# Kernel optimization log

Measured on AMD Instinct MI355X. Metric: run time of the kernel, lower is better.

The kernel has to match this reference:

```python
import jax, jax.numpy as jnp
import numpy as np

T, B, D, H = 512, 64, 1024, 1024  # seq_len, batch, input_dim, hidden (out_dim, bi_dir=False)


def setup_inputs() -> dict:
    key = jax.random.key(0)
    k = jax.random.split(key, 5)
    s = 1.0 / np.sqrt(H)  # PyTorch LSTMCell init scale
    x = jax.random.normal(k[0], (T, B, D), dtype=jnp.float32)
    W_ih = jax.random.uniform(k[1], (4 * H, D), minval=-s, maxval=s, dtype=jnp.float32)
    W_hh = jax.random.uniform(k[2], (4 * H, H), minval=-s, maxval=s, dtype=jnp.float32)
    b_ih = jax.random.uniform(k[3], (4 * H,), minval=-s, maxval=s, dtype=jnp.float32)
    b_hh = jax.random.uniform(k[4], (4 * H,), minval=-s, maxval=s, dtype=jnp.float32)
    return {"x": x, "W_ih": W_ih, "W_hh": W_hh, "b_ih": b_ih, "b_hh": b_hh}


def reference(x, W_ih, W_hh, b_ih, b_hh):
    # Unidirectional LSTM over [T, B, D] -> [T, B, H], PyTorch LSTMCell gate order i,f,g,o.
    # Precompute input contribution for all timesteps in one big GEMM.
    xg = jnp.einsum('tbd,gd->tbg', x, W_ih) + b_ih + b_hh  # [T, B, 4H]

    def step(carry, xg_t):
        h, c = carry
        gates = xg_t + h @ W_hh.T  # [B, 4H]
        i, f, g, o = jnp.split(gates, 4, axis=-1)
        c = jax.nn.sigmoid(f) * c + jax.nn.sigmoid(i) * jnp.tanh(g)
        h = jax.nn.sigmoid(o) * jnp.tanh(c)
        return (h, c), h

    h0 = jnp.zeros((B, H), dtype=x.dtype)
    c0 = jnp.zeros((B, H), dtype=x.dtype)
    _, hs = jax.lax.scan(step, (h0, c0), xg)  # hs: [T, B, H]
    return hs
```

## Files before the change

kernel.cpp:

```cpp
#include <hip/hip_runtime.h>
#include <hip/hip_bf16.h>
#include <stdint.h>

#define T_STEPS 512
#define BATCH   64
#define DIM     1024
#define HID     1024
#define NG      4096
#define MROWS   (T_STEPS * BATCH)

typedef __bf16 bf16;
typedef __bf16 bf16x4 __attribute__((ext_vector_type(4)));
typedef __bf16 bf16x8 __attribute__((ext_vector_type(8)));
typedef float  f32x4  __attribute__((ext_vector_type(4)));
typedef unsigned int u32;
typedef u32 u32x2 __attribute__((ext_vector_type(2)));
typedef u32 u32x4 __attribute__((ext_vector_type(4)));

__device__ __forceinline__ void g2lds16(const void* g, void* l) {
    __builtin_amdgcn_global_load_lds(
        (const __attribute__((address_space(1))) void*)g,
        (__attribute__((address_space(3))) void*)l, 16, 0, 0);
}

__device__ __forceinline__ float fsigmoid(float x) {
    return 1.0f / (1.0f + __expf(-x));
}
__device__ __forceinline__ float ftanh_(float x) {
    return 1.0f - 2.0f / (__expf(2.0f * x) + 1.0f);
}

__device__ __forceinline__ u32x4 load16_cc(const void* p) {
    u32x4 r;
    asm volatile("global_load_dwordx4 %0, %1, off sc0 sc1" : "=v"(r) : "v"(p) : "memory");
    return r;
}
__device__ __forceinline__ void store2_cc(void* p, u32 v) {
    asm volatile("global_store_short %0, %1, off sc0 sc1" :: "v"(p), "v"(v) : "memory");
}
__device__ __forceinline__ u32x2 load8_cached(const void* p) {
    u32x2 r;
    asm volatile("global_load_dwordx2 %0, %1, off" : "=v"(r) : "v"(p) : "memory");
    return r;
}
__device__ __forceinline__ void store4_f32(float* p, float v) {
    asm volatile("global_store_dword %0, %1, off" :: "v"(p), "v"(v) : "memory");
}
#define WAITVM(n) asm volatile("s_waitcnt vmcnt(" #n ")" ::: "memory")

__global__ __launch_bounds__(256) void prep_kernel(
    const float* __restrict__ x,   const float* __restrict__ wih,
    const float* __restrict__ whh, const float* __restrict__ bih,
    const float* __restrict__ bhh,
    bf16* __restrict__ xb, bf16* __restrict__ wihp, bf16* __restrict__ wfrag,
    float* __restrict__ bsump, bf16* __restrict__ hbuf, u32* __restrict__ flags)
{
    const int nt  = gridDim.x * blockDim.x;
    const int gid = blockIdx.x * blockDim.x + threadIdx.x;

    for (int i = gid; i < MROWS * DIM / 4; i += nt) {
        f32x4 v = *(const f32x4*)(x + (size_t)i * 4);
        bf16x4 o = {(bf16)v[0], (bf16)v[1], (bf16)v[2], (bf16)v[3]};
        *(bf16x4*)(xb + (size_t)i * 4) = o;
    }
    for (int i = gid; i < NG * (DIM / 4); i += nt) {
        const int n = i >> 8, c4 = (i & 255) * 4;
        f32x4 v = *(const f32x4*)(wih + (size_t)n * DIM + c4);
        bf16x4 o = {(bf16)v[0], (bf16)v[1], (bf16)v[2], (bf16)v[3]};
        const int np = ((n & 1023) << 2) | (n >> 10);
        *(bf16x4*)(wihp + (size_t)np * DIM + c4) = o;
    }
    for (int i = gid; i < NG * HID / 8; i += nt) {
        const int lane = i & 63;
        const int f    = (i >> 6) & 63;
        const int wv   = (i >> 12) & 3;
        const int hg   = i >> 14;
        const int n = f & 7, kk = f >> 3;
        const int grow = (lane & 3) * 1024 + hg * 32 + n * 4 + ((lane & 15) >> 2);
        const int k0   = wv * 256 + kk * 32 + (lane >> 4) * 8;
        f32x4 v0 = *(const f32x4*)(whh + (size_t)grow * HID + k0);
        f32x4 v1 = *(const f32x4*)(whh + (size_t)grow * HID + k0 + 4);
        bf16x8 o = {(bf16)v0[0], (bf16)v0[1], (bf16)v0[2], (bf16)v0[3],
                    (bf16)v1[0], (bf16)v1[1], (bf16)v1[2], (bf16)v1[3]};
        *(bf16x8*)(wfrag + (size_t)i * 8) = o;
    }
    for (int i = gid; i < NG; i += nt)
        bsump[((i & 1023) << 2) | (i >> 10)] = bih[i] + bhh[i];
    for (int i = gid; i < BATCH * HID / 4; i += nt) {
        bf16x4 z = {(bf16)0.f, (bf16)0.f, (bf16)0.f, (bf16)0.f};
        *(bf16x4*)(hbuf + (size_t)i * 4) = z;
    }
    for (int i = gid; i < 256 * 16; i += nt)
        flags[i] = 0u;
}

__global__ __launch_bounds__(256) void gemm_kernel(
    const bf16* __restrict__ A, const bf16* __restrict__ B,
    const float* __restrict__ bsum, bf16* __restrict__ xgp)
{
    __shared__ char lds[16384];
    char* As = lds;
    char* Bs = lds + 8192;

    const int tid  = threadIdx.x;
    const int lane = tid & 63;
    const int wv   = tid >> 6;
    const int wr   = wv >> 1, wc = wv & 1;
    const int bx   = blockIdx.x & 31;
    const int by   = blockIdx.x >> 5;
    const int m0   = by * 128, n0 = bx * 128;

    f32x4 acc[4][4] = {};

    const int r4 = tid >> 2;
    const int c8 = (tid & 3) * 8;
    const size_t arow0 = (size_t)(m0 +      r4) * DIM + c8;
    const size_t arow1 = (size_t)(m0 + 64 + r4) * DIM + c8;
    const size_t brow0 = (size_t)(n0 +      r4) * DIM + c8;
    const size_t brow1 = (size_t)(n0 + 64 + r4) * DIM + c8;
    const int ldsoff = tid * 16;

    for (int k0 = 0; k0 < DIM; k0 += 32) {
        g2lds16(A + arow0 + k0, As + ldsoff);
        g2lds16(A + arow1 + k0, As + 4096 + ldsoff);
        g2lds16(B + brow0 + k0, Bs + ldsoff);
        g2lds16(B + brow1 + k0, Bs + 4096 + ldsoff);
        __syncthreads();

        bf16x8 af[4], bfr[4];
        #pragma unroll
        for (int i = 0; i < 4; ++i) {
            af[i]  = *(const bf16x8*)(As + (wr*64 + i*16 + (lane & 15))*64 + (lane >> 4)*16);
            bfr[i] = *(const bf16x8*)(Bs + (wc*64 + i*16 + (lane & 15))*64 + (lane >> 4)*16);
        }
        #pragma unroll
        for (int i = 0; i < 4; ++i)
            #pragma unroll
            for (int j = 0; j < 4; ++j)
                acc[i][j] = __builtin_amdgcn_mfma_f32_16x16x32_bf16(
                    af[i], bfr[j], acc[i][j], 0, 0, 0);
        __syncthreads();
    }

    #pragma unroll
    for (int j = 0; j < 4; ++j) {
        const int nn = n0 + wc*64 + j*16 + (lane & 15);
        const float bias = bsum[nn];
        #pragma unroll
        for (int i = 0; i < 4; ++i) {
            #pragma unroll
            for (int r = 0; r < 4; ++r) {
                const int mm = m0 + wr*64 + i*16 + ((lane >> 4) << 2) + r;
                xgp[(size_t)mm * NG + nn] = (bf16)(acc[i][j][r] + bias);
            }
        }
    }
}

__global__ __launch_bounds__(256, 1) void lstm_kernel(
    const bf16* __restrict__ xgp, const bf16* __restrict__ wfrag,
    bf16* __restrict__ hbuf, u32* __restrict__ flags, float* __restrict__ out)
{
    __shared__ float gbuf[4][8][136];

    const int tid  = threadIdx.x;
    const int lane = tid & 63;
    const int wv   = tid >> 6;
    const int wg   = blockIdx.x;
    const int hg   = wg & 31;
    const int bg   = wg >> 5;

    bf16x8 wreg[64];
    {
        const bf16* wb = wfrag + ((size_t)(hg * 4 + wv) * 4096 + lane) * 8;
        #pragma unroll
        for (int f = 0; f < 64; ++f)
            wreg[f] = *(const bf16x8*)(wb + (size_t)f * 512);
    }

    const int frow  = lane & 15;
    const int hrow  = bg * 8 + (frow & 7);
    const int kbase = wv * 256 + (lane >> 4) * 8;
    const int b_el  = tid >> 5;
    const int j_el  = tid & 31;
    const int hid   = hg * 32 + j_el;

    const u32* pollp = flags + ((bg * 32 + wv * 8 + (lane & 7)) << 4);
    u32* myflag      = flags + ((bg * 32 + hg) << 4);

    float c = 0.f;
    float hv_prev = 0.f;
    u32x2 xr = load8_cached(xgp + (size_t)(bg * 8 + b_el) * NG + hid * 4);

    #pragma unroll 1
    for (int step = 0; step < T_STEPS; ++step) {
        while (__hip_atomic_load(pollp, __ATOMIC_RELAXED,
                                 __HIP_MEMORY_SCOPE_AGENT) < (u32)step)
            __builtin_amdgcn_s_sleep(1);

        const bf16* hb = hbuf + (step & 1) * (BATCH * HID) + (size_t)hrow * HID + kbase;
        u32x4 afr[8];
        #pragma unroll
        for (int kk = 0; kk < 8; ++kk)
            afr[kk] = load16_cc(hb + kk * 32);

        const int orow = (step == 0) ? 0 : step - 1;
        store4_f32(out + (size_t)(orow * BATCH + bg * 8 + b_el) * HID + hid, hv_prev);
        u32x2 xr_n = xr;
        if (step + 1 < T_STEPS)
            xr_n = load8_cached(xgp + ((size_t)((step + 1) * BATCH) + bg * 8 + b_el) * NG
                                    + hid * 4);
        WAITVM(2);
        __builtin_amdgcn_sched_barrier(0);

        f32x4 acc[8] = {};
        #pragma unroll
        for (int kk = 0; kk < 8; ++kk) {
            bf16x8 a = __builtin_bit_cast(bf16x8, afr[kk]);
            #pragma unroll
            for (int n = 0; n < 8; ++n)
                acc[n] = __builtin_amdgcn_mfma_f32_16x16x32_bf16(
                    a, wreg[kk * 8 + n], acc[n], 0, 0, 0);
        }

        if (lane < 32) {
            const int q = lane >> 4;
            #pragma unroll
            for (int n = 0; n < 8; ++n)
                #pragma unroll
                for (int r = 0; r < 4; ++r)
                    gbuf[wv][q * 4 + r][n * 16 + frow] = acc[n][r];
        }
        __syncthreads();

        bf16x4 xv = __builtin_bit_cast(bf16x4, xr);
        float P[4];
        #pragma unroll
        for (int g = 0; g < 4; ++g)
            P[g] = gbuf[0][b_el][j_el * 4 + g] + gbuf[1][b_el][j_el * 4 + g]
                 + gbuf[2][b_el][j_el * 4 + g] + gbuf[3][b_el][j_el * 4 + g]
                 + (float)xv[g];
        const float ig = fsigmoid(P[0]);
        const float fg = fsigmoid(P[1]);
        const float gg = ftanh_(P[2]);
        const float og = fsigmoid(P[3]);
        c = fg * c + ig * gg;
        const float hv = og * ftanh_(c);

        const bf16 h16 = (bf16)hv;
        store2_cc(hbuf + ((step & 1) ^ 1) * (BATCH * HID)
                       + (size_t)(bg * 8 + b_el) * HID + hid,
                  (u32)__builtin_bit_cast(unsigned short, h16));
        WAITVM(0);
        __builtin_amdgcn_sched_barrier(0);
        __syncthreads();
        if (tid == 0)
            __hip_atomic_store(myflag, (u32)(step + 1),
                               __ATOMIC_RELAXED, __HIP_MEMORY_SCOPE_AGENT);
        hv_prev = hv;
        xr = xr_n;
    }

    store4_f32(out + (size_t)((T_STEPS - 1) * BATCH + bg * 8 + b_el) * HID + hid,
               hv_prev);
}

extern "C" void kernel_launch(void* const* d_in, const int* in_sizes, int n_in,
                              void* d_out, int out_size, void* d_ws, size_t ws_size,
                              hipStream_t stream) {
    const float* x   = (const float*)d_in[0];
    const float* wih = (const float*)d_in[1];
    const float* whh = (const float*)d_in[2];
    const float* bih = (const float*)d_in[3];
    const float* bhh = (const float*)d_in[4];
    float* out = (float*)d_out;

    char* ws = (char*)d_ws;
    size_t off = 0;
    bf16* xgp   = (bf16*)(ws + off); off += (size_t)MROWS * NG * 2;
    bf16* xb    = (bf16*)(ws + off); off += (size_t)MROWS * DIM * 2;
    bf16* wihp  = (bf16*)(ws + off); off += (size_t)NG * DIM * 2;
    bf16* wfrag = (bf16*)(ws + off); off += (size_t)NG * HID * 2;
    float* bsum = (float*)(ws + off); off += (size_t)NG * 4;
    bf16* hbuf  = (bf16*)(ws + off); off += (size_t)2 * BATCH * HID * 2;
    u32* flags  = (u32*)(ws + off); off += 256 * 16 * 4;
    (void)ws_size; (void)in_sizes; (void)n_in; (void)out_size;

    prep_kernel<<<2048, 256, 0, stream>>>(x, wih, whh, bih, bhh,
                                          xb, wihp, wfrag, bsum, hbuf, flags);
    gemm_kernel<<<8192, 256, 0, stream>>>(xb, wihp, bsum, xgp);
    lstm_kernel<<<256, 256, 0, stream>>>(xgp, wfrag, hbuf, flags, out);
}
```

Baseline: 2.141 ms.

## Split h-state wait into two halves, stage h via LDS, remap GEMM blocks

The LSTM step now polls the flags for the first half of the hidden-chunk producers, loads that half of h, then polls the second half. It runs the first four MFMA k-slices while the second half is still in flight. Hidden-state loads are coalesced row-wise and staged through a padded LDS buffer before being read as MFMA fragments. The GEMM block index is also permuted across groups of 8 to change the block-to-tile assignment, presumably for cache or XCD locality. There is a risk of LDS hazards: the hstage writes and reads have no barrier, which relies on each wave reading only its own slice.

Result: faster. 1.974 ms (-7.8%).

```diff
diff --git a/kernel.cpp b/kernel.cpp
--- a/kernel.cpp
+++ b/kernel.cpp
@@ -106,8 +106,9 @@
     const int lane = tid & 63;
     const int wv   = tid >> 6;
     const int wr   = wv >> 1, wc = wv & 1;
-    const int bx   = blockIdx.x & 31;
-    const int by   = blockIdx.x >> 5;
+    const int wgid = (blockIdx.x & 7) * 1024 + (blockIdx.x >> 3);
+    const int bx   = wgid & 31;
+    const int by   = wgid >> 5;
     const int m0   = by * 128, n0 = bx * 128;
 
     f32x4 acc[4][4] = {};
@@ -161,6 +162,7 @@
     const bf16* __restrict__ xgp, const bf16* __restrict__ wfrag,
     bf16* __restrict__ hbuf, u32* __restrict__ flags, float* __restrict__ out)
 {
+    __shared__ char  hstage[8 * 2064];
     __shared__ float gbuf[4][8][136];
 
     const int tid  = threadIdx.x;
@@ -179,14 +181,18 @@
     }
 
     const int frow  = lane & 15;
-    const int hrow  = bg * 8 + (frow & 7);
-    const int kbase = wv * 256 + (lane >> 4) * 8;
     const int b_el  = tid >> 5;
     const int j_el  = tid & 31;
     const int hid   = hg * 32 + j_el;
 
-    const u32* pollp = flags + ((bg * 32 + wv * 8 + (lane & 7)) << 4);
-    u32* myflag      = flags + ((bg * 32 + hg) << 4);
+    const int goff = (lane >> 3) * 2048 + wv * 512 + (lane & 7) * 16;
+    const int woff = (lane >> 3) * 2064 + wv * 512 + (lane & 7) * 16;
+    const int rbase = frow & 7;
+    const int cbase = rbase * 2064 + wv * 512 + (lane >> 4) * 16;
+
+    const u32* pollpA = flags + ((bg * 32 + wv * 8 + (lane & 3)) << 4);
+    const u32* pollpB = flags + ((bg * 32 + wv * 8 + 4 + (lane & 3)) << 4);
+    u32* myflag       = flags + ((bg * 32 + hg) << 4);
 
     float c = 0.f;
     float hv_prev = 0.f;
@@ -194,29 +200,46 @@
 
     #pragma unroll 1
     for (int step = 0; step < T_STEPS; ++step) {
-        while (__hip_atomic_load(pollp, __ATOMIC_RELAXED,
+        while (__hip_atomic_load(pollpA, __ATOMIC_RELAXED,
                                  __HIP_MEMORY_SCOPE_AGENT) < (u32)step)
             __builtin_amdgcn_s_sleep(1);
 
-        const bf16* hb = hbuf + (step & 1) * (BATCH * HID) + (size_t)hrow * HID + kbase;
-        u32x4 afr[8];
-        #pragma unroll
-        for (int kk = 0; kk < 8; ++kk)
-            afr[kk] = load16_cc(hb + kk * 32);
-
+        const char* hbp = (const char*)(hbuf + (step & 1) * (BATCH * HID)
+                                             + (size_t)(bg * 8) * HID);
+        u32x4 s0 = load16_cc(hbp + goff);
+        u32x4 s1 = load16_cc(hbp + goff + 128);
+
+        while (__hip_atomic_load(pollpB, __ATOMIC_RELAXED,
+                                 __HIP_MEMORY_SCOPE_AGENT) < (u32)step)
+            __builtin_amdgcn_s_sleep(1);
+
+        u32x4 s2 = load16_cc(hbp + goff + 256);
+        u32x4 s3 = load16_cc(hbp + goff + 384);
         const int orow = (step == 0) ? 0 : step - 1;
         store4_f32(out + (size_t)(orow * BATCH + bg * 8 + b_el) * HID + hid, hv_prev);
-        u32x2 xr_n = xr;
-        if (step + 1 < T_STEPS)
-            xr_n = load8_cached(xgp + ((size_t)((step + 1) * BATCH) + bg * 8 + b_el) * NG
-                                    + hid * 4);
+        const int nx = (step + 1 < T_STEPS) ? step + 1 : step;
+        u32x2 xr_n = load8_cached(xgp + ((size_t)(nx * BATCH) + bg * 8 + b_el) * NG
+                                      + hid * 4);
+
+        *(u32x4*)(hstage + woff)       = s0;
+        *(u32x4*)(hstage + woff + 128) = s1;
+        f32x4 acc[8] = {};
+        #pragma unroll
+        for (int kk = 0; kk < 4; ++kk) {
+            bf16x8 a = *(const bf16x8*)(hstage + cbase + kk * 64);
+            #pragma unroll
+            for (int n = 0; n < 8; ++n)
+                acc[n] = __builtin_amdgcn_mfma_f32_16x16x32_bf16(
+                    a, wreg[kk * 8 + n], acc[n], 0, 0, 0);
+        }
+
         WAITVM(2);
         __builtin_amdgcn_sched_barrier(0);
-
-        f32x4 acc[8] = {};
-        #pragma unroll
-        for (int kk = 0; kk < 8; ++kk) {
-            bf16x8 a = __builtin_bit_cast(bf16x8, afr[kk]);
+        *(u32x4*)(hstage + woff + 256) = s2;
+        *(u32x4*)(hstage + woff + 384) = s3;
+        #pragma unroll
+        for (int kk = 4; kk < 8; ++kk) {
+            bf16x8 a = *(const bf16x8*)(hstage + cbase + kk * 64);
             #pragma unroll
             for (int n = 0; n < 8; ++n)
                 acc[n] = __builtin_amdgcn_mfma_f32_16x16x32_bf16(
```
